# Performance work log

Hardware: AMD Instinct MI355X
Metric: run time of the kernel (lower is better)

Reference implementation:

```python
import jax, jax.numpy as jnp
import numpy as np

N_NODES = 100000   # n_user (70k) + m_item (30k)
N_EDGES = 2000000  # bidirectional user-item interaction edges
DIM = 64           # latent_dim = config['recdim']


def setup_inputs() -> dict:
    key = jax.random.key(0)
    k1, k2, k3, k4 = jax.random.split(key, 4)
    x = jax.random.normal(k1, (N_NODES, DIM), dtype=jnp.float32)
    edge_index = jax.random.randint(k2, (2, N_EDGES), 0, N_NODES, dtype=jnp.int32)
    # w_linears: Linear(2*D, D) per layer; stored as [in, out] so y = h @ W + b
    s = 1.0 / np.sqrt(2 * DIM)
    W0 = jax.random.normal(k3, (2 * DIM, DIM), dtype=jnp.float32) * s
    b0 = jnp.zeros((DIM,), dtype=jnp.float32)
    W1 = jax.random.normal(k4, (2 * DIM, DIM), dtype=jnp.float32) * s
    b1 = jnp.zeros((DIM,), dtype=jnp.float32)
    return {"x": x, "edge_index": edge_index, "W0": W0, "b0": b0, "W1": W1, "b1": b1}


def reference(x, edge_index, W0, b0, W1, b1):
    # SAGE-style: neighbor gather + mean aggregation + concat(self, agg) + per-layer linear
    n = x.shape[0]
    src = edge_index[0]  # message source nodes
    dst = edge_index[1]  # message destination nodes
    deg = jax.ops.segment_sum(jnp.ones(src.shape[0], x.dtype), dst, num_segments=n)
    inv_deg = (1.0 / jnp.maximum(deg, 1.0))[:, None]  # [N,1] mean normalizer

    h = x
    layers = ((W0, b0, True), (W1, b1, False))
    for W, b, apply_relu in layers:
        agg = jax.ops.segment_sum(h[src], dst, num_segments=n) * inv_deg  # [N,D] neighbor mean
        h = jnp.concatenate([h, agg], axis=1) @ W + b                      # [N,2D] @ [2D,D]
        if apply_relu:
            h = jax.nn.relu(h)
    return h
```

## Files before the change

kernel.cpp:

```cpp
#include <hip/hip_runtime.h>
#include <hip/hip_bf16.h>

#define N_NODES 100000
#define N_EDGES 2000000
#define DIM 64
#define NB 391
#define CAP 8192
#define PCAP 8192
#define EPB 4096
#define EPT 16
#define BIN_BLOCKS ((N_EDGES + EPB - 1) / EPB)
#define XCONV_BLOCKS (N_NODES * DIM / 4 / 256)
#define LSTRIDE 144

typedef __attribute__((ext_vector_type(8))) short short8;
typedef __attribute__((ext_vector_type(4))) float f32x4;
typedef __attribute__((ext_vector_type(2))) float f32x2;

__global__ __launch_bounds__(256) void binprep_kernel(const int* __restrict__ src,
                                                      const int* __restrict__ dst,
                                                      int* __restrict__ gbcur,
                                                      int* __restrict__ ebuf,
                                                      const float* __restrict__ x,
                                                      uint2* __restrict__ xb4,
                                                      int* __restrict__ xf8,
                                                      const float* __restrict__ W0,
                                                      const float* __restrict__ W1,
                                                      __hip_bfloat16* __restrict__ wfrag) {
    __shared__ int buf[EPB];
    __shared__ short bufb[EPB];
    __shared__ int a[512];
    __shared__ int lscan[NB], lcur[NB], gbase[NB];

    const int bid = blockIdx.x;
    if (bid >= BIN_BLOCKS) {
        const int pb = bid - BIN_BLOCKS;
        if (pb < XCONV_BLOCKS) {
            const int i = pb * 256 + threadIdx.x;
            const float4 v = ((const float4*)x)[i];
            __hip_bfloat162 p0 = __float22bfloat162_rn(make_float2(v.x, v.y));
            __hip_bfloat162 p1 = __float22bfloat162_rn(make_float2(v.z, v.w));
            uint2 ob;
            ob.x = *(unsigned int*)&p0;
            ob.y = *(unsigned int*)&p1;
            xb4[i] = ob;
            int w = __builtin_amdgcn_cvt_pk_fp8_f32(v.x, v.y, 0, false);
            w = __builtin_amdgcn_cvt_pk_fp8_f32(v.z, v.w, w, true);
            xf8[i] = w;
            if (pb == 0 && threadIdx.x < 16) xf8[N_NODES * 16 + threadIdx.x] = 0;
        } else {
            const int tid = (pb - XCONV_BLOCKS) * 256 + threadIdx.x;
            const int j    = tid & 7;
            const int lane = (tid >> 3) & 63;
            const int kc   = (tid >> 9) & 3;
            const int nt   = (tid >> 11) & 3;
            const int l    = tid >> 13;
            const int k = kc * 32 + (lane >> 4) * 8 + j;
            const int n = nt * 16 + (lane & 15);
            const float* W = l ? W1 : W0;
            wfrag[tid] = __float2bfloat16(W[k * 64 + n]);
        }
        return;
    }

    const int t = threadIdx.x;
    const int e0 = bid * EPB;
    const int cnt = min(EPB, N_EDGES - e0);

    for (int i = t; i < 512; i += 256) a[i] = 0;
    __syncthreads();

    int ls[EPT], ld[EPT];
    #pragma unroll
    for (int k = 0; k < EPT; ++k) {
        const int o = t + k * 256;
        if (o < cnt) {
            ls[k] = src[e0 + o];
            ld[k] = dst[e0 + o];
            atomicAdd(&a[ld[k] >> 8], 1);
        } else ld[k] = -1;
    }
    __syncthreads();

    #pragma unroll
    for (int d = 1; d < 512; d <<= 1) {
        const int idx = (t + 1) * 2 * d - 1;
        if (idx < 512) a[idx] += a[idx - d];
        __syncthreads();
    }
    if (t == 0) a[511] = 0;
    __syncthreads();
    #pragma unroll
    for (int d = 256; d >= 1; d >>= 1) {
        const int idx = (t + 1) * 2 * d - 1;
        if (idx < 512) {
            const int tmp = a[idx - d];
            a[idx - d] = a[idx];
            a[idx] += tmp;
        }
        __syncthreads();
    }
    for (int i = t; i < NB; i += 256) {
        const int c = a[i + 1] - a[i];
        lscan[i] = a[i];
        lcur[i]  = a[i];
        gbase[i] = c ? atomicAdd(&gbcur[i], c) : 0;
    }
    __syncthreads();

    #pragma unroll
    for (int k = 0; k < EPT; ++k) {
        if (ld[k] >= 0) {
            const int b = ld[k] >> 8;
            const int p = atomicAdd(&lcur[b], 1);
            buf[p]  = (ls[k] << 8) | (ld[k] & 255);
            bufb[p] = (short)b;
        }
    }
    __syncthreads();
    for (int i = t; i < cnt; i += 256) {
        const int pk = buf[i];
        const int b  = bufb[i];
        ebuf[b * CAP + gbase[b] + (i - lscan[b])] = pk;
    }
}

__global__ __launch_bounds__(256) void fillpass_kernel(const int* __restrict__ ebuf,
                                                       const int* __restrict__ gbcur,
                                                       int2* __restrict__ nodeinfo,
                                                       int* __restrict__ csr) {
    __shared__ int cnt[256];
    __shared__ int s[256];
    __shared__ int cur[256];
    const int b = blockIdx.x;
    const int t = threadIdx.x;
    const int nbase = b << 8;
    const int ecnt = gbcur[b];
    const int estart = b * CAP;

    cnt[t] = 0;
    __syncthreads();
    for (int i = t; i < ecnt; i += 256)
        atomicAdd(&cnt[ebuf[estart + i] & 255], 1);
    __syncthreads();

    const int deg  = cnt[t];
    const int pdeg = (deg + 3) & ~3;
    s[t] = pdeg;
    __syncthreads();
    #pragma unroll
    for (int off = 1; off < 256; off <<= 1) {
        int u = (t >= off) ? s[t - off] : 0;
        __syncthreads();
        s[t] += u;
        __syncthreads();
    }
    const int rp = b * PCAP + s[t] - pdeg;
    if (nbase + t < N_NODES) nodeinfo[nbase + t] = make_int2(rp, deg);
    cur[t] = rp;
    __syncthreads();

    for (int i = t; i < ecnt; i += 256) {
        const int pk = ebuf[estart + i];
        const int p = atomicAdd(&cur[pk & 255], 1);
        csr[p] = pk >> 8;
    }
    __syncthreads();
    for (int p = rp + deg; p < rp + pdeg; ++p)
        csr[p] = N_NODES;
}

template <bool RELU, bool OUTF32, bool WRF8>
__global__ __launch_bounds__(256) void sage_fused_kernel(
        const uint2* __restrict__ f8tbl,
        const unsigned short* __restrict__ hb,
        const int2* __restrict__ nodeinfo,
        const uint4* __restrict__ csr4,
        const unsigned short* __restrict__ wfrag,
        const float* __restrict__ bias,
        float* __restrict__ outf,
        unsigned short* __restrict__ outb,
        unsigned char* __restrict__ outf8) {
    __shared__ __align__(16) unsigned char aggL[64 * LSTRIDE];

    const int tid = threadIdx.x;
    const int base = blockIdx.x * 64;

    {
        const int g = tid >> 3;
        const int r = tid & 7;

        #define CONSUME(u, A)                                                 \
            {                                                                 \
                f32x2 f01 = __builtin_amdgcn_cvt_pk_f32_fp8((u).x, false);    \
                f32x2 f23 = __builtin_amdgcn_cvt_pk_f32_fp8((u).x, true);     \
                f32x2 f45 = __builtin_amdgcn_cvt_pk_f32_fp8((u).y, false);    \
                f32x2 f67 = __builtin_amdgcn_cvt_pk_f32_fp8((u).y, true);     \
                A[0] += f01.x; A[1] += f01.y; A[2] += f23.x; A[3] += f23.y;   \
                A[4] += f45.x; A[5] += f45.y; A[6] += f67.x; A[7] += f67.y;   \
            }

        #pragma unroll
        for (int half = 0; half < 2; ++half) {
            const int ln = half * 32 + g;
            const int node = base + ln;
            int2 ni = (node < N_NODES) ? nodeinfo[node] : make_int2(0, 0);
            const int c0 = ni.x >> 2;
            const int deg = ni.y;
            const int rounds = (deg + 3) >> 2;

            float acc[8] = {0.f, 0.f, 0.f, 0.f, 0.f, 0.f, 0.f, 0.f};
            for (int t = 0; t < rounds; ++t) {
                const uint4 id = csr4[c0 + t];
                const uint2 u0 = f8tbl[(size_t)id.x * 8 + r];
                const uint2 u1 = f8tbl[(size_t)id.y * 8 + r];
                const uint2 u2 = f8tbl[(size_t)id.z * 8 + r];
                const uint2 u3 = f8tbl[(size_t)id.w * 8 + r];
                CONSUME(u0, acc); CONSUME(u1, acc); CONSUME(u2, acc); CONSUME(u3, acc);
            }
            const float inv = 1.0f / fmaxf((float)deg, 1.0f);
            __hip_bfloat162 p0 = __float22bfloat162_rn(make_float2(acc[0] * inv, acc[1] * inv));
            __hip_bfloat162 p1 = __float22bfloat162_rn(make_float2(acc[2] * inv, acc[3] * inv));
            __hip_bfloat162 p2 = __float22bfloat162_rn(make_float2(acc[4] * inv, acc[5] * inv));
            __hip_bfloat162 p3 = __float22bfloat162_rn(make_float2(acc[6] * inv, acc[7] * inv));
            uint4 ov;
            ov.x = *(unsigned int*)&p0;
            ov.y = *(unsigned int*)&p1;
            ov.z = *(unsigned int*)&p2;
            ov.w = *(unsigned int*)&p3;
            *(uint4*)(aggL + ln * LSTRIDE + r * 16) = ov;
        }
        #undef CONSUME
    }
    __syncthreads();

    {
        const int wave = tid >> 6;
        const int lane = tid & 63;
        const int m0 = base + wave * 16;
        const int quad = lane >> 4;
        const int lrow = lane & 15;
        const int m = min(m0 + lrow, N_NODES - 1);
        const int ln = wave * 16 + lrow;

        short8 bf[4][4];
        #pragma unroll
        for (int nt = 0; nt < 4; ++nt)
            #pragma unroll
            for (int kc = 0; kc < 4; ++kc)
                bf[nt][kc] = *(const short8*)(wfrag + (size_t)((nt * 4 + kc) * 64 + lane) * 8);

        f32x4 acc[4];
        #pragma unroll
        for (int nt = 0; nt < 4; ++nt) acc[nt] = f32x4{0.f, 0.f, 0.f, 0.f};

        #pragma unroll
        for (int kc = 0; kc < 4; ++kc) {
            short8 af;
            if (kc < 2) {
                af = *(const short8*)(hb + (size_t)m * 64 + kc * 32 + quad * 8);
            } else {
                af = *(const short8*)(aggL + ln * LSTRIDE + (kc - 2) * 64 + quad * 16);
            }
            #pragma unroll
            for (int nt = 0; nt < 4; ++nt)
                acc[nt] = __builtin_amdgcn_mfma_f32_16x16x32_bf16(af, bf[nt][kc], acc[nt], 0, 0, 0);
        }

        #pragma unroll
        for (int nt = 0; nt < 4; ++nt) {
            const float bv = bias[nt * 16 + lrow];
            #pragma unroll
            for (int r = 0; r < 4; ++r) {
                const int mr = m0 + quad * 4 + r;
                if (mr < N_NODES) {
                    float v = acc[nt][r] + bv;
                    if (RELU) v = fmaxf(v, 0.f);
                    const size_t off = (size_t)mr * 64 + nt * 16 + lrow;
                    if (OUTF32) {
                        outf[off] = v;
                    } else {
                        __hip_bfloat16 hv = __float2bfloat16(v);
                        outb[off] = *(unsigned short*)&hv;
                    }
                    if (WRF8) {
                        const int w8 = __builtin_amdgcn_cvt_pk_fp8_f32(v, v, 0, false);
                        outf8[off] = (unsigned char)(w8 & 0xff);
                    }
                }
            }
        }
        if (WRF8 && blockIdx.x == 0 && tid < 8)
            ((unsigned long long*)(outf8 + (size_t)N_NODES * DIM))[tid] = 0ULL;
    }
}

extern "C" void kernel_launch(void* const* d_in, const int* in_sizes, int n_in,
                              void* d_out, int out_size, void* d_ws, size_t ws_size,
                              hipStream_t stream) {
    const float* x  = (const float*)d_in[0];
    const int*   ei = (const int*)d_in[1];
    const float* W0 = (const float*)d_in[2];
    const float* b0 = (const float*)d_in[3];
    const float* W1 = (const float*)d_in[4];
    const float* b1 = (const float*)d_in[5];
    float* out = (float*)d_out;

    const int* src = ei;
    const int* dst = ei + N_EDGES;

    char* ws = (char*)d_ws;
    auto alloc = [&](size_t bytes) {
        char* p = ws;
        ws += (bytes + 255) & ~(size_t)255;
        return p;
    };
    int*  gbcur    = (int*)alloc((size_t)NB * 4);
    int2* nodeinfo = (int2*)alloc((size_t)N_NODES * 8);
    int*  ebuf     = (int*)alloc((size_t)NB * CAP * 4);
    int*  csr      = (int*)alloc((size_t)NB * PCAP * 4);
    unsigned short* xb   = (unsigned short*)alloc((size_t)N_NODES * DIM * 2);
    unsigned char*  xf8  = (unsigned char*)alloc((size_t)(N_NODES + 1) * DIM);
    unsigned short* h1b  = (unsigned short*)alloc((size_t)N_NODES * DIM * 2);
    unsigned char*  h1f8 = (unsigned char*)alloc((size_t)(N_NODES + 1) * DIM);
    __hip_bfloat16* wfrag = (__hip_bfloat16*)alloc((size_t)2 * 8192 * 2);

    hipMemsetAsync(gbcur, 0, (size_t)NB * 4, stream);

    binprep_kernel<<<BIN_BLOCKS + XCONV_BLOCKS + 64, 256, 0, stream>>>(
        src, dst, gbcur, ebuf, x, (uint2*)xb, (int*)xf8, W0, W1, wfrag);
    fillpass_kernel<<<NB, 256, 0, stream>>>(ebuf, gbcur, nodeinfo, csr);

    const int fused_blocks = (N_NODES + 63) / 64;

    sage_fused_kernel<true, false, true><<<fused_blocks, 256, 0, stream>>>(
        (const uint2*)xf8, xb, nodeinfo, (const uint4*)csr,
        (const unsigned short*)wfrag, b0, nullptr, h1b, h1f8);

    sage_fused_kernel<false, true, false><<<fused_blocks, 256, 0, stream>>>(
        (const uint2*)h1f8, h1b, nodeinfo, (const uint4*)csr,
        (const unsigned short*)wfrag + 8192, b1, out, nullptr, nullptr);
}
```

Measured before the change: 211.5 us.

## Use 512-thread fused blocks with one node per thread group and split MFMA columns

The fused SAGE kernel now runs 512 threads per block, so each 8-lane group gathers one node instead of looping over two. The MFMA stage splits the 64 output columns across two wave halves, which halves each wave's B fragments and accumulators. The aim is more independent gathers in flight and fewer registers per thread, at the cost of larger blocks. Separately, the binning kernel now loads 16 contiguous src/dst edges per thread with int4 vector loads instead of strided scalar loads, which changes each thread's edge assignment but should keep results the same.

```diff
diff --git a/kernel.cpp b/kernel.cpp
--- a/kernel.cpp
+++ b/kernel.cpp
@@ -71,15 +71,27 @@
     __syncthreads();
 
     int ls[EPT], ld[EPT];
-    #pragma unroll
-    for (int k = 0; k < EPT; ++k) {
-        const int o = t + k * 256;
-        if (o < cnt) {
-            ls[k] = src[e0 + o];
-            ld[k] = dst[e0 + o];
-            atomicAdd(&a[ld[k] >> 8], 1);
-        } else ld[k] = -1;
-    }
+    const bool act = (t * 16) < cnt;
+    {
+        const int4* s4 = (const int4*)(src + e0 + t * 16);
+        const int4* d4 = (const int4*)(dst + e0 + t * 16);
+        #pragma unroll
+        for (int k = 0; k < 4; ++k) {
+            if (act) {
+                const int4 sv = s4[k];
+                const int4 dv = d4[k];
+                ls[4 * k + 0] = sv.x; ld[4 * k + 0] = dv.x;
+                ls[4 * k + 1] = sv.y; ld[4 * k + 1] = dv.y;
+                ls[4 * k + 2] = sv.z; ld[4 * k + 2] = dv.z;
+                ls[4 * k + 3] = sv.w; ld[4 * k + 3] = dv.w;
+            } else {
+                ld[4 * k + 0] = ld[4 * k + 1] = ld[4 * k + 2] = ld[4 * k + 3] = -1;
+            }
+        }
+    }
+    #pragma unroll
+    for (int k = 0; k < EPT; ++k)
+        if (ld[k] >= 0) atomicAdd(&a[ld[k] >> 8], 1);
     __syncthreads();
 
     #pragma unroll
@@ -171,7 +183,7 @@
 }
 
 template <bool RELU, bool OUTF32, bool WRF8>
-__global__ __launch_bounds__(256) void sage_fused_kernel(
+__global__ __launch_bounds__(512) void sage_fused_kernel(
         const uint2* __restrict__ f8tbl,
         const unsigned short* __restrict__ hb,
         const int2* __restrict__ nodeinfo,
@@ -189,70 +201,72 @@
     {
         const int g = tid >> 3;
         const int r = tid & 7;
-
-        #define CONSUME(u, A)                                                 \
+        const int node = base + g;
+        const int2 ni = (node < N_NODES) ? nodeinfo[node] : make_int2(0, 0);
+        const int c0 = ni.x >> 2;
+        const int deg = ni.y;
+        const int rounds = (deg + 3) >> 2;
+
+        float a0 = 0.f, a1 = 0.f, a2 = 0.f, a3 = 0.f;
+        float a4 = 0.f, a5 = 0.f, a6 = 0.f, a7 = 0.f;
+
+        #define CONSUME(u)                                                    \
             {                                                                 \
                 f32x2 f01 = __builtin_amdgcn_cvt_pk_f32_fp8((u).x, false);    \
                 f32x2 f23 = __builtin_amdgcn_cvt_pk_f32_fp8((u).x, true);     \
                 f32x2 f45 = __builtin_amdgcn_cvt_pk_f32_fp8((u).y, false);    \
                 f32x2 f67 = __builtin_amdgcn_cvt_pk_f32_fp8((u).y, true);     \
-                A[0] += f01.x; A[1] += f01.y; A[2] += f23.x; A[3] += f23.y;   \
-                A[4] += f45.x; A[5] += f45.y; A[6] += f67.x; A[7] += f67.y;   \
+                a0 += f01.x; a1 += f01.y; a2 += f23.x; a3 += f23.y;           \
+                a4 += f45.x; a5 += f45.y; a6 += f67.x; a7 += f67.y;           \
             }
 
-        #pragma unroll
-        for (int half = 0; half < 2; ++half) {
-            const int ln = half * 32 + g;
-            const int node = base + ln;
-            int2 ni = (node < N_NODES) ? nodeinfo[node] : make_int2(0, 0);
-            const int c0 = ni.x >> 2;
-            const int deg = ni.y;
-            const int rounds = (deg + 3) >> 2;
-
-            float acc[8] = {0.f, 0.f, 0.f, 0.f, 0.f, 0.f, 0.f, 0.f};
-            for (int t = 0; t < rounds; ++t) {
-                const uint4 id = csr4[c0 + t];
-                const uint2 u0 = f8tbl[(size_t)id.x * 8 + r];
-                const uint2 u1 = f8tbl[(size_t)id.y * 8 + r];
-                const uint2 u2 = f8tbl[(size_t)id.z * 8 + r];
-                const uint2 u3 = f8tbl[(size_t)id.w * 8 + r];
-                CONSUME(u0, acc); CONSUME(u1, acc); CONSUME(u2, acc); CONSUME(u3, acc);
-            }
-            const float inv = 1.0f / fmaxf((float)deg, 1.0f);
-            __hip_bfloat162 p0 = __float22bfloat162_rn(make_float2(acc[0] * inv, acc[1] * inv));
-            __hip_bfloat162 p1 = __float22bfloat162_rn(make_float2(acc[2] * inv, acc[3] * inv));
-            __hip_bfloat162 p2 = __float22bfloat162_rn(make_float2(acc[4] * inv, acc[5] * inv));
-            __hip_bfloat162 p3 = __float22bfloat162_rn(make_float2(acc[6] * inv, acc[7] * inv));
-            uint4 ov;
-            ov.x = *(unsigned int*)&p0;
-            ov.y = *(unsigned int*)&p1;
-            ov.z = *(unsigned int*)&p2;
-            ov.w = *(unsigned int*)&p3;
-            *(uint4*)(aggL + ln * LSTRIDE + r * 16) = ov;
+        for (int t = 0; t < rounds; ++t) {
+            const uint4 id = csr4[c0 + t];
+            const uint2 u0 = f8tbl[(size_t)id.x * 8 + r];
+            const uint2 u1 = f8tbl[(size_t)id.y * 8 + r];
+            const uint2 u2 = f8tbl[(size_t)id.z * 8 + r];
+            const uint2 u3 = f8tbl[(size_t)id.w * 8 + r];
+            CONSUME(u0); CONSUME(u1); CONSUME(u2); CONSUME(u3);
         }
         #undef CONSUME
+
+        const float inv = 1.0f / fmaxf((float)deg, 1.0f);
+        __hip_bfloat162 p0 = __float22bfloat162_rn(make_float2(a0 * inv, a1 * inv));
+        __hip_bfloat162 p1 = __float22bfloat162_rn(make_float2(a2 * inv, a3 * inv));
+        __hip_bfloat162 p2 = __float22bfloat162_rn(make_float2(a4 * inv, a5 * inv));
+        __hip_bfloat162 p3 = __float22bfloat162_rn(make_float2(a6 * inv, a7 * inv));
+        uint4 ov;
+        ov.x = *(unsigned int*)&p0;
+        ov.y = *(unsigned int*)&p1;
+        ov.z = *(unsigned int*)&p2;
+        ov.w = *(unsigned int*)&p3;
+        *(uint4*)(aggL + g * LSTRIDE + r * 16) = ov;
     }
     __syncthreads();
 
     {
         const int wave = tid >> 6;
         const int lane = tid & 63;
-        const int m0 = base + wave * 16;
+        const int mtile = wave & 3;
+        const int nh = wave >> 2;
+        const int m0 = base + mtile * 16;
         const int quad = lane >> 4;
         const int lrow = lane & 15;
         const int m = min(m0 + lrow, N_NODES - 1);
-        const int ln = wave * 16 + lrow;
-
-        short8 bf[4][4];
-        #pragma unroll
-        for (int nt = 0; nt < 4; ++nt)
+        const int ln = mtile * 16 + lrow;
+
+        short8 bf[2][4];
+        #pragma unroll
+        for (int n2 = 0; n2 < 2; ++n2) {
+            const int nt = nh * 2 + n2;
             #pragma unroll
             for (int kc = 0; kc < 4; ++kc)
-                bf[nt][kc] = *(const short8*)(wfrag + (size_t)((nt * 4 + kc) * 64 + lane) * 8);
-
-        f32x4 acc[4];
-        #pragma unroll
-        for (int nt = 0; nt < 4; ++nt) acc[nt] = f32x4{0.f, 0.f, 0.f, 0.f};
+                bf[n2][kc] = *(const short8*)(wfrag + (size_t)((nt * 4 + kc) * 64 + lane) * 8);
+        }
+
+        f32x4 acc[2];
+        #pragma unroll
+        for (int n2 = 0; n2 < 2; ++n2) acc[n2] = f32x4{0.f, 0.f, 0.f, 0.f};
 
         #pragma unroll
         for (int kc = 0; kc < 4; ++kc) {
@@ -263,18 +277,19 @@
                 af = *(const short8*)(aggL + ln * LSTRIDE + (kc - 2) * 64 + quad * 16);
             }
             #pragma unroll
-            for (int nt = 0; nt < 4; ++nt)
-                acc[nt] = __builtin_amdgcn_mfma_f32_16x16x32_bf16(af, bf[nt][kc], acc[nt], 0, 0, 0);
-        }
-
-        #pragma unroll
-        for (int nt = 0; nt < 4; ++nt) {
+            for (int n2 = 0; n2 < 2; ++n2)
+                acc[n2] = __builtin_amdgcn_mfma_f32_16x16x32_bf16(af, bf[n2][kc], acc[n2], 0, 0, 0);
+        }
+
+        #pragma unroll
+        for (int n2 = 0; n2 < 2; ++n2) {
+            const int nt = nh * 2 + n2;
             const float bv = bias[nt * 16 + lrow];
             #pragma unroll
             for (int r = 0; r < 4; ++r) {
                 const int mr = m0 + quad * 4 + r;
                 if (mr < N_NODES) {
-                    float v = acc[nt][r] + bv;
+                    float v = acc[n2][r] + bv;
                     if (RELU) v = fmaxf(v, 0.f);
                     const size_t off = (size_t)mr * 64 + nt * 16 + lrow;
                     if (OUTF32) {
@@ -333,11 +348,11 @@
 
     const int fused_blocks = (N_NODES + 63) / 64;
 
-    sage_fused_kernel<true, false, true><<<fused_blocks, 256, 0, stream>>>(
+    sage_fused_kernel<true, false, true><<<fused_blocks, 512, 0, stream>>>(
         (const uint2*)xf8, xb, nodeinfo, (const uint4*)csr,
         (const unsigned short*)wfrag, b0, nullptr, h1b, h1f8);
 
-    sage_fused_kernel<false, true, false><<<fused_blocks, 256, 0, stream>>>(
+    sage_fused_kernel<false, true, false><<<fused_blocks, 512, 0, stream>>>(
         (const uint2*)h1f8, h1b, nodeinfo, (const uint4*)csr,
         (const unsigned short*)wfrag + 8192, b1, out, nullptr, nullptr);
 }
```

New measurement: 205.0 us. 1.03x faster.
